# Kernel tuning notes

Hardware: AMD Instinct MI355X
Metric: run time of the kernel (lower is better)

The kernel has to match this reference:

```python
import jax, jax.numpy as jnp
import numpy as np

T, B, N = 12, 2, 1024
M = B * N            # nodes per timestep (batch-flattened)
D_IN, D_H, D_T, D_O = 64, 128, 16, 32


def _linear_params(k, fin, fout):
    kw, kb = jax.random.split(k)
    s = 1.0 / np.sqrt(fin)
    w = jax.random.uniform(kw, (fin, fout), jnp.float32, -s, s)
    b = jax.random.uniform(kb, (fout,), jnp.float32, -s, s)
    return w, b


def setup_inputs() -> dict:
    key = jax.random.key(0)
    ks = jax.random.split(key, 12)
    x = jax.random.normal(ks[0], (T, M, D_IN), jnp.float32)
    A = (jax.random.uniform(ks[1], (T, M, M)) < 0.01).astype(jnp.float32)
    A = A * (1.0 - jnp.eye(M, dtype=jnp.float32))  # no self-loops in raw adjacency
    ego_mask = jax.random.randint(ks[2], (B, T, N), 0, 2).astype(bool)
    gcn1_w, gcn1_b = _linear_params(ks[3], D_IN, D_H)
    gcn2_w, gcn2_b = _linear_params(ks[4], D_H, D_H)
    time_w, time_b = _linear_params(ks[5], 1, D_T)
    q_w, q_b = _linear_params(ks[6], D_H + D_T, D_H)
    k_w, k_b = _linear_params(ks[7], D_H + D_T, D_H)
    v_w, v_b = _linear_params(ks[8], D_H + D_T, D_H)
    o_w, o_b = _linear_params(ks[9], D_H, D_H)
    fc_w, fc_b = _linear_params(ks[10], D_H, D_O)
    return dict(x=x, A=A, ego_mask=ego_mask,
                gcn1_w=gcn1_w, gcn1_b=gcn1_b, gcn2_w=gcn2_w, gcn2_b=gcn2_b,
                time_w=time_w, time_b=time_b,
                q_w=q_w, q_b=q_b, k_w=k_w, k_b=k_b, v_w=v_w, v_b=v_b,
                o_w=o_w, o_b=o_b, fc_w=fc_w, fc_b=fc_b)


def _forward(x, A, ego_mask, gcn1_w, gcn1_b, gcn2_w, gcn2_b, time_w, time_b,
             q_w, q_b, k_w, k_b, v_w, v_b, o_w, o_b, fc_w, fc_b):
    # [B,T,N] -> [T, B*N], as in mask.permute(1,0,2).reshape(T,-1)
    mask = ego_mask.transpose(1, 0, 2).reshape(T, M)
    tvals = jnp.arange(T, dtype=jnp.float32)

    def step(_, inp):
        xt, At, mt, tv = inp  # [M,D_IN], [M,M], [M] bool, scalar
        m = mt.astype(xt.dtype)
        # restrict adjacency to masked subgraph; GCNConv adds self-loops
        A_hat = At * (m[:, None] * m[None, :]) + jnp.diag(m)
        deg = A_hat.sum(axis=0)  # in-degree per target (PyG gcn_norm on col)
        nrm = jnp.where(deg > 0, 1.0 / jnp.sqrt(jnp.maximum(deg, 1e-12)), 0.0)

        def gcn(h, w, b):
            # out[i] = nrm[i] * sum_j A_hat[j,i] * nrm[j] * (hW)[j] + b
            return (A_hat.T @ ((h @ w) * nrm[:, None])) * nrm[:, None] + b

        h = jax.nn.relu(gcn(xt, gcn1_w, gcn1_b))
        h = jax.nn.relu(gcn(h, gcn2_w, gcn2_b))
        # t_vec = sin(Linear(1,D_T)(t)) -- identical for all nodes
        t_vec = jnp.sin(tv * time_w[0] + time_b)  # [D_T]
        xtc = jnp.concatenate([h, jnp.broadcast_to(t_vec, (M, D_T))], axis=-1)
        Q = xtc @ q_w + q_b
        K = xtc @ k_w + k_b
        V = xtc @ v_w + v_b
        scores = (Q @ K.T) * (1.0 / np.sqrt(D_H))  # [M,M]
        scores = jnp.where(mt[None, :], scores, -1e9)  # keys restricted to mask
        agg = jax.nn.softmax(scores, axis=-1) @ V
        out = ((agg @ o_w + o_b) @ fc_w + fc_b) * m[:, None]  # scatter-back == mask
        return None, out

    _, outs = jax.lax.scan(step, None, (x, A, mask, tvals))  # [T,M,D_O]
    return outs.reshape(T, B, N, D_O).transpose(1, 2, 0, 3)  # [B,N,T,D_O]


def reference(x, A, ego_mask, gcn1_w, gcn1_b, gcn2_w, gcn2_b, time_w, time_b,
              q_w, q_b, k_w, k_b, v_w, v_b, o_w, o_b, fc_w, fc_b):
    return _forward(x, A, ego_mask, gcn1_w, gcn1_b, gcn2_w, gcn2_b, time_w,
                    time_b, q_w, q_b, k_w, k_b, v_w, v_b, o_w, o_b, fc_w, fc_b)
```

## Files before the change

kernel.cpp:

```cpp
#include <hip/hip_runtime.h>
#include <stdint.h>

#define TT   12
#define BB   2
#define NN   1024
#define MM   2048
#define TM   24576
#define DIN  64
#define DH   128
#define DOUT 32
#define CAP  64
#define NSPL 4

typedef __attribute__((ext_vector_type(8))) short short8;
typedef __attribute__((ext_vector_type(4))) short short4v;
typedef __attribute__((ext_vector_type(4))) float f32x4;

#define MFMA(a,b,c) __builtin_amdgcn_mfma_f32_16x16x32_bf16((a),(b),(c),0,0,0)

__device__ __forceinline__ float bf2f(unsigned short u){
  union { uint32_t i; float f; } x; x.i = ((uint32_t)u) << 16; return x.f;
}
__device__ __forceinline__ unsigned short f2bf(float f){
  union { float f; uint32_t i; } x; x.f = f;
  uint32_t u = x.i + 0x7FFFu + ((x.i >> 16) & 1u);
  return (unsigned short)(u >> 16);
}
__device__ __forceinline__ float LD(const void* p, size_t i, int mode){
  return mode ? ((const float*)p)[i] : bf2f(((const unsigned short*)p)[i]);
}

__global__ void k_fill(float* __restrict__ out, int n, float val){
  int i = blockIdx.x*blockDim.x + threadIdx.x;
  if(i < n) out[i] = val;
}

__global__ void k_dtype(const unsigned short* __restrict__ x, int* __restrict__ dtf,
                        int* __restrict__ nact){
  __shared__ int cnt_s;
  if(threadIdx.x==0) cnt_s = 0;
  if(threadIdx.x < TT) nact[threadIdx.x] = 0;
  __syncthreads();
  int c = 0;
  for(int i=threadIdx.x; i<6144; i+=blockDim.x){
    unsigned short h = x[i*2];
    unsigned e = (h >> 7) & 0xFF;
    if(h==0 || (e >= 0x60 && e <= 0x9F)) c++;
  }
  atomicAdd(&cnt_s, c);
  __syncthreads();
  if(threadIdx.x==0) *dtf = (cnt_s > 4000) ? 0 : 1;
}

__global__ void k_detect(const unsigned char* __restrict__ p, int* __restrict__ flag){
  __shared__ int pres_s, ge2_s;
  if(threadIdx.x==0){ pres_s=0; ge2_s=0; }
  __syncthreads();
  int pres=0, ge2=0;
  for(int i=threadIdx.x; i<24576; i+=blockDim.x){
    unsigned v = p[i];
    if(v){ pres |= 1 << (i & 7); if(v >= 2u) ge2 = 1; }
  }
  if(pres) atomicOr(&pres_s, pres);
  if(ge2)  atomicOr(&ge2_s, 1);
  __syncthreads();
  if(threadIdx.x==0){
    int pr = pres_s, g2 = ge2_s, mode;
    if(!g2){
      if((pr & ~0x01) == 0)      mode = 4;
      else if((pr & ~0x11) == 0) mode = 0;
      else                       mode = 1;
    } else {
      if((pr & ~0xC0) == 0)      mode = 5;
      else if((pr & ~0xCC) == 0) mode = 3;
      else                       mode = 2;
    }
    *flag = mode;
  }
}

__global__ void k_mask(const void* __restrict__ egom, const int* __restrict__ flag,
                       int* __restrict__ cnt, int* __restrict__ nact,
                       int* __restrict__ aidx, int* __restrict__ inv){
  int idx = blockIdx.x*blockDim.x + threadIdx.x;
  int t = idx / MM, node = idx % MM;
  int b = node / NN, n = node % NN;
  int src = (b*TT + t)*NN + n;
  int mode = *flag;
  int v;
  if(mode==0)      v = ((const int*)egom)[src] != 0;
  else if(mode==1) v = ((const unsigned char*)egom)[src] != 0;
  else if(mode==2) v = ((const unsigned short*)egom)[src] != 0;
  else if(mode==3) v = ((const float*)egom)[src] != 0.f;
  else if(mode==4) v = ((const long long*)egom)[src] != 0;
  else             v = ((const double*)egom)[src] != 0.0;
  cnt[idx] = 0;
  unsigned long long bal = __ballot(v != 0);
  int lane = threadIdx.x & 63;
  int base = 0;
  if(lane == 0 && bal) base = atomicAdd(&nact[t], __popcll(bal));
  base = __shfl(base, 0, 64);
  int ic = -1;
  if(v){
    int pfx = __popcll(bal & ((1ULL << lane) - 1ULL));
    ic = base + pfx;
    aidx[(size_t)t*MM + ic] = node;
  }
  inv[idx] = ic;
}

__global__ void k_conv(const void* __restrict__ x, const int* __restrict__ dtf,
                       const int* __restrict__ nact, const int* __restrict__ aidx,
                       unsigned short* __restrict__ xc){
  int id = blockIdx.x*blockDim.x + threadIdx.x;
  int rowc = id >> 3, seg = id & 7;
  int t = rowc / MM, ic = rowc % MM;
  int na = nact[t];
  if(ic >= ((na+63)&~63)) return;
  short8 o = {0,0,0,0,0,0,0,0};
  if(ic < na){
    int node = aidx[(size_t)t*MM + ic];
    size_t src = ((size_t)t*MM + node)*DIN + seg*8;
    if(*dtf){
      const float4* xf = (const float4*)((const float*)x + src);
      float4 a = xf[0], b = xf[1];
      o[0]=(short)f2bf(a.x); o[1]=(short)f2bf(a.y); o[2]=(short)f2bf(a.z); o[3]=(short)f2bf(a.w);
      o[4]=(short)f2bf(b.x); o[5]=(short)f2bf(b.y); o[6]=(short)f2bf(b.z); o[7]=(short)f2bf(b.w);
    } else {
      o = *(const short8*)((const unsigned short*)x + src);
    }
  }
  *(short8*)(xc + (size_t)rowc*DIN + seg*8) = o;
}

__global__ void k_prepw(
  const void* __restrict__ w1, const void* __restrict__ w2,
  const void* __restrict__ qw, const void* __restrict__ kw, const void* __restrict__ vw,
  const void* __restrict__ qb0, const void* __restrict__ kb0, const void* __restrict__ vb0,
  const void* __restrict__ ow, const void* __restrict__ ob,
  const void* __restrict__ fw, const void* __restrict__ fb,
  const void* __restrict__ tw, const void* __restrict__ tb,
  const void* __restrict__ b1, const void* __restrict__ b2,
  const int* __restrict__ dtf,
  unsigned short* __restrict__ W1t, unsigned short* __restrict__ W2t,
  unsigned short* __restrict__ Wqt, unsigned short* __restrict__ Wkt,
  unsigned short* __restrict__ Wvt, unsigned short* __restrict__ Wct,
  float* __restrict__ qbf, float* __restrict__ kbf, float* __restrict__ vbf,
  float* __restrict__ bcf, float* __restrict__ b1f, float* __restrict__ b2f)
{
  const int md = *dtf;
  int id = blockIdx.x*blockDim.x + threadIdx.x;
  if(id < 8192){ int n=id/64, k2=id%64; W1t[n*64+k2]=f2bf(LD(w1,(size_t)k2*128+n,md)); return; }
  id -= 8192;
  if(id < 16384){ int n=id/128,k2=id%128; W2t[n*128+k2]=f2bf(LD(w2,(size_t)k2*128+n,md)); return; }
  id -= 16384;
  if(id < 16384){ int n=id/128,k2=id%128; Wqt[n*128+k2]=f2bf(LD(qw,(size_t)k2*128+n,md)); return; }
  id -= 16384;
  if(id < 16384){ int n=id/128,k2=id%128; Wkt[n*128+k2]=f2bf(LD(kw,(size_t)k2*128+n,md)); return; }
  id -= 16384;
  if(id < 16384){ int n=id/128,k2=id%128; Wvt[n*128+k2]=f2bf(LD(vw,(size_t)k2*128+n,md)); return; }
  id -= 16384;
  if(id < 4096){
    int oc=id/128, c=id%128; float s=0.f;
    for(int r=0;r<128;r++) s += LD(ow,(size_t)c*128+r,md)*LD(fw,(size_t)r*32+oc,md);
    Wct[oc*128+c]=f2bf(s); return;
  }
  id -= 4096;
  if(id < 32){
    float s = LD(fb,id,md);
    for(int r=0;r<128;r++) s += LD(ob,r,md)*LD(fw,(size_t)r*32+id,md);
    bcf[id]=s; return;
  }
  id -= 32;
  if(id < 4608){
    int which = id/1536, rem=id%1536, t=rem/128, n=rem%128;
    const void* W  = which==0?qw:(which==1?kw:vw);
    const void* Bs = which==0?qb0:(which==1?kb0:vb0);
    float s = LD(Bs,n,md);
    for(int d=0;d<16;d++){
      float tv = sinf((float)t*LD(tw,d,md) + LD(tb,d,md));
      s += tv * LD(W,(size_t)(128+d)*128+n,md);
    }
    float* dst = which==0?qbf:(which==1?kbf:vbf);
    dst[t*128+n]=s; return;
  }
  id -= 4608;
  if(id < 256){
    if(id<128) b1f[id] = LD(b1,id,md);
    else       b2f[id-128] = LD(b2,id-128,md);
    return;
  }
}

__global__ __launch_bounds__(256) void k_edges(const void* __restrict__ A,
    const int* __restrict__ dtf, const int* __restrict__ inv,
    int* __restrict__ cnt, int* __restrict__ edges){
  int id = blockIdx.x*blockDim.x + threadIdx.x;
  int seg = id & 63; int row = id >> 6;
  int t = row / MM;
  int jc = inv[row];
  if(jc < 0) return;
  const int* invt = inv + (size_t)t*MM;
  int* cb = cnt + (size_t)t*MM;
  int* eb = edges + (size_t)t*MM*CAP;
  if(*dtf){
    const float4* p4 = (const float4*)((const float*)A + (size_t)row*MM + seg*32);
    #pragma unroll
    for(int u=0;u<8;u++){
      float4 v = p4[u];
      float wd[4]={v.x,v.y,v.z,v.w};
      #pragma unroll
      for(int q=0;q<4;q++){
        if(wd[q]!=0.f){
          int ibc = invt[seg*32 + u*4 + q];
          if(ibc >= 0){ int s=atomicAdd(&cb[ibc],1); if(s<CAP) eb[(size_t)ibc*CAP+s]=jc; }
        }
      }
    }
  } else {
    const uint4* p4 = (const uint4*)((const unsigned short*)A + (size_t)row*MM + seg*32);
    #pragma unroll
    for(int u=0;u<4;u++){
      uint4 v = p4[u];
      unsigned wd[4]={v.x,v.y,v.z,v.w};
      #pragma unroll
      for(int q=0;q<4;q++){
        int ib = seg*32 + u*8 + q*2;
        if(wd[q] & 0xFFFFu){
          int ibc = invt[ib];
          if(ibc >= 0){ int s=atomicAdd(&cb[ibc],1); if(s<CAP) eb[(size_t)ibc*CAP+s]=jc; }
        }
        if(wd[q] >> 16){
          int ibc = invt[ib+1];
          if(ibc >= 0){ int s=atomicAdd(&cb[ibc],1); if(s<CAP) eb[(size_t)ibc*CAP+s]=jc; }
        }
      }
    }
  }
}

template<int KD>
__global__ __launch_bounds__(256) void k_gemm_f32(const unsigned short* __restrict__ X,
    const unsigned short* __restrict__ Wt, float* __restrict__ g,
    const int* __restrict__ nact)
{
  constexpr int KS = KD/32;
  const int tile = blockIdx.x*64;
  const int t = tile / MM, il = tile % MM;
  const int na = nact[t];
  if(il >= ((na+63)&~63)) return;
  const int tid=threadIdx.x, wv=tid>>6, lane=tid&63, l15=lane&15, quad=lane>>4;
  const int r0 = tile + (wv>>1)*32;
  const int c0 = (wv&1)*64;
  short8 bf[KS][4];
  #pragma unroll
  for(int kk=0;kk<KS;kk++)
    #pragma unroll
    for(int nt=0;nt<4;nt++)
      bf[kk][nt] = *(const short8*)(Wt + (size_t)(c0+nt*16+l15)*KD + kk*32 + quad*8);
  f32x4 z = {0.f,0.f,0.f,0.f};
  f32x4 acc[2][4];
  #pragma unroll
  for(int i=0;i<2;i++){ acc[i][0]=z; acc[i][1]=z; acc[i][2]=z; acc[i][3]=z; }
  #pragma unroll
  for(int kk=0;kk<KS;kk++){
    short8 a0 = *(const short8*)(X + (size_t)(r0+l15)*KD    + kk*32 + quad*8);
    short8 a1 = *(const short8*)(X + (size_t)(r0+16+l15)*KD + kk*32 + quad*8);
    #pragma unroll
    for(int nt=0;nt<4;nt++){
      acc[0][nt]=MFMA(a0,bf[kk][nt],acc[0][nt]);
      acc[1][nt]=MFMA(a1,bf[kk][nt],acc[1][nt]);
    }
  }
  #pragma unroll
  for(int mt=0;mt<2;mt++)
    #pragma unroll
    for(int nt=0;nt<4;nt++){
      int col = c0+nt*16+l15;
      #pragma unroll
      for(int r=0;r<4;r++){
        int row = r0 + mt*16 + quad*4 + r;
        g[(size_t)row*DH + col] = acc[mt][nt][r];
      }
    }
}

__global__ __launch_bounds__(256) void k_gather(const float* __restrict__ g,
    const int* __restrict__ edges, const int* __restrict__ cnt,
    const int* __restrict__ nact, const float* __restrict__ bias,
    unsigned short* __restrict__ h)
{
  int wv = threadIdx.x>>6, lane = threadIdx.x&63;
  int gi = blockIdx.x*4 + wv;
  int t = gi / MM, ic = gi % MM;
  int na = nact[t];
  if(ic >= ((na+63)&~63)) return;
  if(ic >= na){
    h[(size_t)gi*DH + lane] = 0; h[(size_t)gi*DH + 64 + lane] = 0;
    return;
  }
  float a0=0.f, a1=0.f;
  int cn = cnt[gi]; if(cn>CAP) cn=CAP;
  const int* eb = edges + (size_t)gi*CAP;
  for(int e=0;e<cn;e++){
    int jc = eb[e];
    float nj = rsqrtf((float)cnt[(size_t)t*MM+jc] + 1.f);
    const float* gr = g + ((size_t)t*MM + jc)*DH;
    a0 += nj*gr[lane]; a1 += nj*gr[64+lane];
  }
  float ni = rsqrtf((float)cn + 1.f);
  const float* gs = g + (size_t)gi*DH;
  float h0 = ni*(a0 + ni*gs[lane])    + bias[lane];
  float h1 = ni*(a1 + ni*gs[64+lane]) + bias[64+lane];
  h0 = h0>0.f?h0:0.f; h1 = h1>0.f?h1:0.f;
  h[(size_t)gi*DH + lane]      = f2bf(h0);
  h[(size_t)gi*DH + 64 + lane] = f2bf(h1);
}

__global__ __launch_bounds__(256) void k_gemm_qkv(const unsigned short* __restrict__ X,
    const unsigned short* __restrict__ Wq, const unsigned short* __restrict__ Wk,
    const unsigned short* __restrict__ Wv,
    const float* __restrict__ qb, const float* __restrict__ kb, const float* __restrict__ vb,
    unsigned short* __restrict__ Qo, unsigned short* __restrict__ Ko,
    unsigned short* __restrict__ Vr, const int* __restrict__ nact)
{
  const int tile = blockIdx.x*64;
  const int t = tile / MM, il = tile % MM;
  const int na = nact[t];
  if(il >= ((na+63)&~63)) return;
  const int which = blockIdx.z;
  const unsigned short* Wt = which==0?Wq:(which==1?Wk:Wv);
  const float* bias = which==0?qb:(which==1?kb:vb);
  unsigned short* o = which==0?Qo:(which==1?Ko:Vr);
  const int tid=threadIdx.x, wv=tid>>6, lane=tid&63, l15=lane&15, quad=lane>>4;
  const int r0 = tile + (wv>>1)*32;
  const int c0 = (wv&1)*64;
  short8 bf[4][4];
  #pragma unroll
  for(int kk=0;kk<4;kk++)
    #pragma unroll
    for(int nt=0;nt<4;nt++)
      bf[kk][nt] = *(const short8*)(Wt + (size_t)(c0+nt*16+l15)*DH + kk*32 + quad*8);
  f32x4 z = {0.f,0.f,0.f,0.f};
  f32x4 acc[2][4];
  #pragma unroll
  for(int i=0;i<2;i++){ acc[i][0]=z; acc[i][1]=z; acc[i][2]=z; acc[i][3]=z; }
  #pragma unroll
  for(int kk=0;kk<4;kk++){
    short8 a0 = *(const short8*)(X + (size_t)(r0+l15)*DH    + kk*32 + quad*8);
    short8 a1 = *(const short8*)(X + (size_t)(r0+16+l15)*DH + kk*32 + quad*8);
    #pragma unroll
    for(int nt=0;nt<4;nt++){
      acc[0][nt]=MFMA(a0,bf[kk][nt],acc[0][nt]);
      acc[1][nt]=MFMA(a1,bf[kk][nt],acc[1][nt]);
    }
  }
  #pragma unroll
  for(int mt=0;mt<2;mt++)
    #pragma unroll
    for(int nt=0;nt<4;nt++){
      int col = c0+nt*16+l15;
      float bb = bias[t*DH+col];
      #pragma unroll
      for(int r=0;r<4;r++){
        int row = r0 + mt*16 + quad*4 + r;
        o[(size_t)row*DH + col] = f2bf(acc[mt][nt][r] + bb);
      }
    }
}

__global__ __launch_bounds__(64) void k_vtrans(const unsigned short* __restrict__ Vr,
    const int* __restrict__ nact, unsigned short* __restrict__ Vtc)
{
  __shared__ unsigned short tl[64][130];
  const int i0 = blockIdx.x*64, t = blockIdx.y, l = threadIdx.x;
  const int na = nact[t];
  if(i0 >= ((na+63)&~63)) return;
  for(int r=0;r<64;r++){
    uint32_t vv = *(const uint32_t*)(Vr + ((size_t)t*MM + i0 + r)*DH + 2*l);
    tl[r][2*l]   = (unsigned short)(vv & 0xFFFFu);
    tl[r][2*l+1] = (unsigned short)(vv >> 16);
  }
  __syncthreads();
  for(int c=0;c<DH;c++)
    Vtc[(size_t)t*DH*MM + (size_t)c*MM + i0 + l] = tl[l][c];
}

__global__ __launch_bounds__(64) void k_attn_split(
  const unsigned short* __restrict__ Q, const unsigned short* __restrict__ Kc,
  const unsigned short* __restrict__ Vtc, const int* __restrict__ nact,
  float* __restrict__ part, float* __restrict__ lpart)
{
  __shared__ short Pl[16][72];
  const int lane=threadIdx.x&63, l15=lane&15, quad=lane>>4;
  const int t = blockIdx.y;
  const int qbase = blockIdx.x*16;
  const int z = blockIdx.z;
  const float scale = 0.088388347648318447f;
  const int na = nact[t];
  if(qbase >= na) return;
  const int nkt = (na + 63) >> 6;
  const int chunk = (nkt + NSPL - 1) / NSPL;
  const int kt0 = z*chunk;
  int kt1 = kt0 + chunk; if(kt1 > nkt) kt1 = nkt;

  short8 bq[4];
  #pragma unroll
  for(int kk=0;kk<4;kk++)
    bq[kk] = *(const short8*)(Q + ((size_t)t*MM + qbase + l15)*DH + kk*32 + quad*8);

  f32x4 zz = {0.f,0.f,0.f,0.f};
  f32x4 accPV[8];
  #pragma unroll
  for(int i=0;i<8;i++) accPV[i]=zz;
  float l_run = 0.f;

  for(int kt=kt0; kt<kt1; kt++){
    const int key0 = kt*64;
    #pragma unroll
    for(int mt=0;mt<4;mt++){
      f32x4 s = zz;
      const unsigned short* Krow = Kc + ((size_t)t*MM + key0 + mt*16 + l15)*DH;
      #pragma unroll
      for(int kk=0;kk<4;kk++){
        short8 ak = *(const short8*)(Krow + kk*32 + quad*8);
        s = MFMA(ak, bq[kk], s);
      }
      short4v pk;
      #pragma unroll
      for(int r=0;r<4;r++){
        float sv = fminf(fmaxf(s[r]*scale, -15.f), 15.f);
        float valid = (key0 + mt*16 + quad*4 + r < na) ? 1.f : 0.f;
        float p = __expf(sv) * valid;
        pk[r] = (short)f2bf(p);
        l_run += bf2f((unsigned short)pk[r]);
      }
      *(short4v*)&Pl[l15][mt*16 + quad*4] = pk;
    }
    #pragma unroll
    for(int kk=0;kk<2;kk++){
      short8 ap = *(const short8*)&Pl[l15][kk*32 + quad*8];
      const unsigned short* Vb = Vtc + (size_t)t*DH*MM + key0 + kk*32 + quad*8;
      #pragma unroll
      for(int nt=0;nt<8;nt++){
        short8 bv = *(const short8*)(Vb + (size_t)(nt*16 + l15)*MM);
        accPV[nt] = MFMA(ap, bv, accPV[nt]);
      }
    }
  }
  l_run += __shfl_xor(l_run, 16, 64);
  l_run += __shfl_xor(l_run, 32, 64);

  const size_t pbase = (size_t)(z*TT + t)*MM + qbase;
  #pragma unroll
  for(int nt=0;nt<8;nt++)
    #pragma unroll
    for(int r=0;r<4;r++)
      part[(pbase + quad*4 + r)*128 + nt*16 + l15] = accPV[nt][r];
  if(lane < 16) lpart[pbase + lane] = l_run;
}

__global__ __launch_bounds__(64) void k_attn_fin(
  const float* __restrict__ part, const float* __restrict__ lpart,
  const int* __restrict__ aidx, const int* __restrict__ nact,
  const unsigned short* __restrict__ Wct, const float* __restrict__ bc,
  float* __restrict__ out)
{
  __shared__ short Al[16][136];
  __shared__ float lbuf[16];
  const int lane=threadIdx.x&63, l15=lane&15, quad=lane>>4;
  const int t = blockIdx.y, qbase = blockIdx.x*16;
  const int na = nact[t];
  if(qbase >= na) return;
  f32x4 acc4[8];
  f32x4 zz = {0.f,0.f,0.f,0.f};
  #pragma unroll
  for(int i=0;i<8;i++) acc4[i]=zz;
  #pragma unroll
  for(int s=0;s<NSPL;s++){
    const float* pb = part + ((size_t)(s*TT + t)*MM + qbase)*128;
    #pragma unroll
    for(int i=0;i<8;i++){
      int flat = i*64 + lane;
      int q = flat >> 5, c4 = (flat & 31) << 2;
      acc4[i] += *(const f32x4*)(pb + q*128 + c4);
    }
  }
  if(lane < 16){
    float ls = 0.f;
    #pragma unroll
    for(int s=0;s<NSPL;s++) ls += lpart[(size_t)(s*TT + t)*MM + qbase + lane];
    lbuf[lane] = ls;
  }
  #pragma unroll
  for(int i=0;i<8;i++){
    int flat = i*64 + lane;
    int q = flat >> 5, c4 = (flat & 31) << 2;
    short4v pk;
    #pragma unroll
    for(int r=0;r<4;r++){
      float av = fminf(fmaxf(acc4[i][r], -1e30f), 1e30f);
      pk[r] = (short)f2bf(av);
    }
    *(short4v*)&Al[q][c4] = pk;
  }
  __syncthreads();

  const int qc = qbase + l15;
  const bool qok = (qc < na);
  const float lsv = lbuf[l15];
  const float linv = (lsv > 0.f) ? 1.f/lsv : 0.f;
  const int node = aidx[(size_t)t*MM + (qok ? qc : 0)];
  #pragma unroll
  for(int mt2=0;mt2<2;mt2++){
    f32x4 d = zz;
    #pragma unroll
    for(int kk=0;kk<4;kk++){
      short8 aw = *(const short8*)(Wct + (size_t)(mt2*16+l15)*DH + kk*32 + quad*8);
      short8 bl = *(const short8*)&Al[l15][kk*32 + quad*8];
      d = MFMA(aw, bl, d);
    }
    f32x4 bcv = *(const f32x4*)(bc + mt2*16 + quad*4);
    f32x4 o4;
    #pragma unroll
    for(int r=0;r<4;r++) o4[r] = d[r]*linv + bcv[r];
    if(qok)
      *(f32x4*)(out + (size_t)node*(TT*DOUT) + (size_t)t*DOUT + mt2*16 + quad*4) = o4;
  }
}

extern "C" void kernel_launch(void* const* d_in, const int* in_sizes, int n_in,
                              void* d_out, int out_size, void* d_ws, size_t ws_size,
                              hipStream_t stream)
{
  float* outp = (float*)d_out;
  static const int EXP[19] = {1572864,50331648,24576,8192,128,16384,128,16,16,
                              18432,128,18432,128,18432,128,16384,128,4096,32};
  bool ok = (n_in >= 19) && (out_size == 786432);
  if(ok) for(int i=0;i<19;i++) if(in_sizes[i] != EXP[i]) { ok = false; break; }
  if(!ok){
    k_fill<<<(out_size+255)/256,256,0,stream>>>(outp, out_size, 1000.f);
    return;
  }
  const void* x   = d_in[0];
  const void* A   = d_in[1];
  const void* eg  = d_in[2];
  const void* w1  = d_in[3];
  const void* b1  = d_in[4];
  const void* w2  = d_in[5];
  const void* b2  = d_in[6];
  const void* tw  = d_in[7];
  const void* tb  = d_in[8];
  const void* qw  = d_in[9];
  const void* qb0 = d_in[10];
  const void* kw  = d_in[11];
  const void* kb0 = d_in[12];
  const void* vw  = d_in[13];
  const void* vb0 = d_in[14];
  const void* ow  = d_in[15];
  const void* ob  = d_in[16];
  const void* fw  = d_in[17];
  const void* fb  = d_in[18];

  char* w = (char*)d_ws;
  size_t off = 0;
  auto alloc = [&](size_t sz)->char*{
    char* p = w + off; off = (off + sz + 255) & ~(size_t)255; return p; };
  int*   flag  = (int*)  alloc(4);
  int*   dtf   = (int*)  alloc(4);
  int*   nactb = (int*)  alloc(TT*4);
  int*   cnt   = (int*)  alloc((size_t)TM*4);
  int*   aidx  = (int*)  alloc((size_t)TM*4);
  int*   inv   = (int*)  alloc((size_t)TM*4);
  int*   edges = (int*)  alloc((size_t)TM*CAP*4);
  float* g     = (float*)alloc((size_t)TM*DH*4);
  unsigned short* h   = (unsigned short*)alloc((size_t)TM*DH*2);
  unsigned short* xc  = (unsigned short*)alloc((size_t)TM*DIN*2);
  unsigned short* Vr  = (unsigned short*)alloc((size_t)TM*DH*2);
  unsigned short* Vtc = (unsigned short*)alloc((size_t)TT*DH*MM*2);
  unsigned short* W1t = (unsigned short*)alloc(DH*DIN*2);
  unsigned short* W2t = (unsigned short*)alloc(DH*DH*2);
  unsigned short* Wqt = (unsigned short*)alloc(DH*DH*2);
  unsigned short* Wkt = (unsigned short*)alloc(DH*DH*2);
  unsigned short* Wvt = (unsigned short*)alloc(DH*DH*2);
  unsigned short* Wct = (unsigned short*)alloc(DOUT*DH*2);
  float* qbf = (float*)alloc(TT*DH*4);
  float* kbf = (float*)alloc(TT*DH*4);
  float* vbf = (float*)alloc(TT*DH*4);
  float* bcf = (float*)alloc(DOUT*4);
  float* b1f = (float*)alloc(DH*4);
  float* b2f = (float*)alloc(DH*4);
  float* part  = (float*)alloc((size_t)NSPL*TM*DH*4);
  float* lpart = (float*)alloc((size_t)NSPL*TM*4);
  if(off > ws_size){
    k_fill<<<(out_size+255)/256,256,0,stream>>>(outp, out_size, 500.f);
    return;
  }

  unsigned short* Qb = (unsigned short*)g;
  unsigned short* Kb = (unsigned short*)((char*)g + (size_t)TM*DH*2);

  k_fill<<<(out_size+255)/256,256,0,stream>>>(outp, out_size, 0.f);
  k_dtype<<<1,256,0,stream>>>((const unsigned short*)x, dtf, nactb);
  k_detect<<<1,256,0,stream>>>((const unsigned char*)eg, flag);
  k_mask<<<TM/256,256,0,stream>>>(eg, flag, cnt, nactb, aidx, inv);
  k_conv<<<TM*8/256,256,0,stream>>>(x, dtf, nactb, aidx, xc);
  k_prepw<<<(82720+255)/256,256,0,stream>>>(w1,w2,qw,kw,vw,qb0,kb0,vb0,ow,ob,fw,fb,tw,tb,
                                            b1,b2,dtf,
                                            W1t,W2t,Wqt,Wkt,Wvt,Wct,qbf,kbf,vbf,bcf,b1f,b2f);
  k_edges<<<TM*64/256,256,0,stream>>>(A, dtf, inv, cnt, edges);
  k_gemm_f32<DIN><<<TM/64,256,0,stream>>>(xc, W1t, g, nactb);
  k_gather<<<TM/4,256,0,stream>>>(g, edges, cnt, nactb, b1f, h);
  k_gemm_f32<DH><<<TM/64,256,0,stream>>>(h, W2t, g, nactb);
  k_gather<<<TM/4,256,0,stream>>>(g, edges, cnt, nactb, b2f, h);
  k_gemm_qkv<<<dim3(TM/64,1,3),256,0,stream>>>(h, Wqt,Wkt,Wvt, qbf,kbf,vbf, Qb,Kb,Vr, nactb);
  k_vtrans<<<dim3(MM/64,TT),64,0,stream>>>(Vr, nactb, Vtc);
  k_attn_split<<<dim3(MM/16,TT,NSPL),64,0,stream>>>(Qb, Kb, Vtc, nactb, part, lpart);
  k_attn_fin<<<dim3(MM/16,TT),64,0,stream>>>(part, lpart, aidx, nactb, Wct, bcf, outp);
}
```

Measured before the change: 571.7 us.

## Fuse small prologue kernels and fold gather/transposes into GEMM loads and stores

Merges the dtype and mask-format detection kernels into one two-block launch, and folds the output zero-fill into the mask kernel. The compaction copy (k_conv) is removed by gathering x rows through aidx directly inside the first GEMM. The separate V transpose kernel is removed by having the QKV GEMM write V in transposed layout. The weight-prep index order is also changed so reads of the source weights coalesce. These cut several launches and intermediate buffers, at the cost of uncoalesced strided stores for the transposed V and gathered A-operand loads in the first GEMM.

```diff
diff --git a/kernel.cpp b/kernel.cpp
--- a/kernel.cpp
+++ b/kernel.cpp
@@ -11,6 +11,7 @@
 #define DOUT 32
 #define CAP  64
 #define NSPL 4
+#define OUTSZ 786432
 
 typedef __attribute__((ext_vector_type(8))) short short8;
 typedef __attribute__((ext_vector_type(4))) short short4v;
@@ -29,60 +30,76 @@
 __device__ __forceinline__ float LD(const void* p, size_t i, int mode){
   return mode ? ((const float*)p)[i] : bf2f(((const unsigned short*)p)[i]);
 }
+__device__ __forceinline__ short8 ldx8(const void* x, size_t off, int md){
+  if(md){
+    const float4* xf = (const float4*)((const float*)x + off);
+    float4 a = xf[0], b = xf[1];
+    short8 o;
+    o[0]=(short)f2bf(a.x); o[1]=(short)f2bf(a.y); o[2]=(short)f2bf(a.z); o[3]=(short)f2bf(a.w);
+    o[4]=(short)f2bf(b.x); o[5]=(short)f2bf(b.y); o[6]=(short)f2bf(b.z); o[7]=(short)f2bf(b.w);
+    return o;
+  }
+  return *(const short8*)((const unsigned short*)x + off);
+}
 
 __global__ void k_fill(float* __restrict__ out, int n, float val){
   int i = blockIdx.x*blockDim.x + threadIdx.x;
   if(i < n) out[i] = val;
 }
 
-__global__ void k_dtype(const unsigned short* __restrict__ x, int* __restrict__ dtf,
-                        int* __restrict__ nact){
-  __shared__ int cnt_s;
-  if(threadIdx.x==0) cnt_s = 0;
-  if(threadIdx.x < TT) nact[threadIdx.x] = 0;
-  __syncthreads();
-  int c = 0;
-  for(int i=threadIdx.x; i<6144; i+=blockDim.x){
-    unsigned short h = x[i*2];
-    unsigned e = (h >> 7) & 0xFF;
-    if(h==0 || (e >= 0x60 && e <= 0x9F)) c++;
-  }
-  atomicAdd(&cnt_s, c);
-  __syncthreads();
-  if(threadIdx.x==0) *dtf = (cnt_s > 4000) ? 0 : 1;
-}
-
-__global__ void k_detect(const unsigned char* __restrict__ p, int* __restrict__ flag){
-  __shared__ int pres_s, ge2_s;
-  if(threadIdx.x==0){ pres_s=0; ge2_s=0; }
-  __syncthreads();
-  int pres=0, ge2=0;
-  for(int i=threadIdx.x; i<24576; i+=blockDim.x){
-    unsigned v = p[i];
-    if(v){ pres |= 1 << (i & 7); if(v >= 2u) ge2 = 1; }
-  }
-  if(pres) atomicOr(&pres_s, pres);
-  if(ge2)  atomicOr(&ge2_s, 1);
-  __syncthreads();
-  if(threadIdx.x==0){
-    int pr = pres_s, g2 = ge2_s, mode;
-    if(!g2){
-      if((pr & ~0x01) == 0)      mode = 4;
-      else if((pr & ~0x11) == 0) mode = 0;
-      else                       mode = 1;
-    } else {
-      if((pr & ~0xC0) == 0)      mode = 5;
-      else if((pr & ~0xCC) == 0) mode = 3;
-      else                       mode = 2;
-    }
-    *flag = mode;
+__global__ void k_detect2(const unsigned short* __restrict__ x,
+                          const unsigned char* __restrict__ eg,
+                          int* __restrict__ dtf, int* __restrict__ flag,
+                          int* __restrict__ nact){
+  if(blockIdx.x == 0){
+    __shared__ int cnt_s;
+    if(threadIdx.x==0) cnt_s = 0;
+    if(threadIdx.x < TT) nact[threadIdx.x] = 0;
+    __syncthreads();
+    int c = 0;
+    for(int i=threadIdx.x; i<6144; i+=blockDim.x){
+      unsigned short h = x[i*2];
+      unsigned e = (h >> 7) & 0xFF;
+      if(h==0 || (e >= 0x60 && e <= 0x9F)) c++;
+    }
+    atomicAdd(&cnt_s, c);
+    __syncthreads();
+    if(threadIdx.x==0) *dtf = (cnt_s > 4000) ? 0 : 1;
+  } else {
+    __shared__ int pres_s, ge2_s;
+    if(threadIdx.x==0){ pres_s=0; ge2_s=0; }
+    __syncthreads();
+    int pres=0, ge2=0;
+    for(int i=threadIdx.x; i<24576; i+=blockDim.x){
+      unsigned v = eg[i];
+      if(v){ pres |= 1 << (i & 7); if(v >= 2u) ge2 = 1; }
+    }
+    if(pres) atomicOr(&pres_s, pres);
+    if(ge2)  atomicOr(&ge2_s, 1);
+    __syncthreads();
+    if(threadIdx.x==0){
+      int pr = pres_s, g2 = ge2_s, mode;
+      if(!g2){
+        if((pr & ~0x01) == 0)      mode = 4;
+        else if((pr & ~0x11) == 0) mode = 0;
+        else                       mode = 1;
+      } else {
+        if((pr & ~0xC0) == 0)      mode = 5;
+        else if((pr & ~0xCC) == 0) mode = 3;
+        else                       mode = 2;
+      }
+      *flag = mode;
+    }
   }
 }
 
 __global__ void k_mask(const void* __restrict__ egom, const int* __restrict__ flag,
                        int* __restrict__ cnt, int* __restrict__ nact,
-                       int* __restrict__ aidx, int* __restrict__ inv){
+                       int* __restrict__ aidx, int* __restrict__ inv,
+                       float* __restrict__ out){
   int idx = blockIdx.x*blockDim.x + threadIdx.x;
+  out[idx] = 0.f;
+  if(idx >= TM) return;
   int t = idx / MM, node = idx % MM;
   int b = node / NN, n = node % NN;
   int src = (b*TT + t)*NN + n;
@@ -109,30 +126,6 @@
   inv[idx] = ic;
 }
 
-__global__ void k_conv(const void* __restrict__ x, const int* __restrict__ dtf,
-                       const int* __restrict__ nact, const int* __restrict__ aidx,
-                       unsigned short* __restrict__ xc){
-  int id = blockIdx.x*blockDim.x + threadIdx.x;
-  int rowc = id >> 3, seg = id & 7;
-  int t = rowc / MM, ic = rowc % MM;
-  int na = nact[t];
-  if(ic >= ((na+63)&~63)) return;
-  short8 o = {0,0,0,0,0,0,0,0};
-  if(ic < na){
-    int node = aidx[(size_t)t*MM + ic];
-    size_t src = ((size_t)t*MM + node)*DIN + seg*8;
-    if(*dtf){
-      const float4* xf = (const float4*)((const float*)x + src);
-      float4 a = xf[0], b = xf[1];
-      o[0]=(short)f2bf(a.x); o[1]=(short)f2bf(a.y); o[2]=(short)f2bf(a.z); o[3]=(short)f2bf(a.w);
-      o[4]=(short)f2bf(b.x); o[5]=(short)f2bf(b.y); o[6]=(short)f2bf(b.z); o[7]=(short)f2bf(b.w);
-    } else {
-      o = *(const short8*)((const unsigned short*)x + src);
-    }
-  }
-  *(short8*)(xc + (size_t)rowc*DIN + seg*8) = o;
-}
-
 __global__ void k_prepw(
   const void* __restrict__ w1, const void* __restrict__ w2,
   const void* __restrict__ qw, const void* __restrict__ kw, const void* __restrict__ vw,
@@ -150,18 +143,19 @@
 {
   const int md = *dtf;
   int id = blockIdx.x*blockDim.x + threadIdx.x;
-  if(id < 8192){ int n=id/64, k2=id%64; W1t[n*64+k2]=f2bf(LD(w1,(size_t)k2*128+n,md)); return; }
+  if(id < 8192){
+    int n=id&127, k2=id>>7; W1t[n*64+k2]=f2bf(LD(w1,(size_t)k2*128+n,md)); return; }
   id -= 8192;
-  if(id < 16384){ int n=id/128,k2=id%128; W2t[n*128+k2]=f2bf(LD(w2,(size_t)k2*128+n,md)); return; }
+  if(id < 16384){ int n=id&127,k2=id>>7; W2t[n*128+k2]=f2bf(LD(w2,(size_t)k2*128+n,md)); return; }
   id -= 16384;
-  if(id < 16384){ int n=id/128,k2=id%128; Wqt[n*128+k2]=f2bf(LD(qw,(size_t)k2*128+n,md)); return; }
+  if(id < 16384){ int n=id&127,k2=id>>7; Wqt[n*128+k2]=f2bf(LD(qw,(size_t)k2*128+n,md)); return; }
   id -= 16384;
-  if(id < 16384){ int n=id/128,k2=id%128; Wkt[n*128+k2]=f2bf(LD(kw,(size_t)k2*128+n,md)); return; }
+  if(id < 16384){ int n=id&127,k2=id>>7; Wkt[n*128+k2]=f2bf(LD(kw,(size_t)k2*128+n,md)); return; }
   id -= 16384;
-  if(id < 16384){ int n=id/128,k2=id%128; Wvt[n*128+k2]=f2bf(LD(vw,(size_t)k2*128+n,md)); return; }
+  if(id < 16384){ int n=id&127,k2=id>>7; Wvt[n*128+k2]=f2bf(LD(vw,(size_t)k2*128+n,md)); return; }
   id -= 16384;
   if(id < 4096){
-    int oc=id/128, c=id%128; float s=0.f;
+    int oc=id&31, c=id>>5; float s=0.f;
     for(int r=0;r<128;r++) s += LD(ow,(size_t)c*128+r,md)*LD(fw,(size_t)r*32+oc,md);
     Wct[oc*128+c]=f2bf(s); return;
   }
@@ -239,12 +233,61 @@
   }
 }
 
-template<int KD>
-__global__ __launch_bounds__(256) void k_gemm_f32(const unsigned short* __restrict__ X,
+__global__ __launch_bounds__(256) void k_gemm_x(const void* __restrict__ x,
+    const int* __restrict__ dtf, const int* __restrict__ nact,
+    const int* __restrict__ aidx, const unsigned short* __restrict__ Wt,
+    float* __restrict__ g)
+{
+  const int tile = blockIdx.x*64;
+  const int t = tile / MM, il = tile % MM;
+  const int na = nact[t];
+  if(il >= ((na+63)&~63)) return;
+  const int md = *dtf;
+  const int tid=threadIdx.x, wv=tid>>6, lane=tid&63, l15=lane&15, quad=lane>>4;
+  const int r0 = tile + (wv>>1)*32;
+  const int c0 = (wv&1)*64;
+  short8 bf[2][4];
+  #pragma unroll
+  for(int kk=0;kk<2;kk++)
+    #pragma unroll
+    for(int nt=0;nt<4;nt++)
+      bf[kk][nt] = *(const short8*)(Wt + (size_t)(c0+nt*16+l15)*DIN + kk*32 + quad*8);
+  const int il0 = (r0 % MM) + l15, il1 = (r0 % MM) + 16 + l15;
+  const int n0 = aidx[(size_t)t*MM + (il0 < na ? il0 : 0)];
+  const int n1 = aidx[(size_t)t*MM + (il1 < na ? il1 : 0)];
+  const size_t xb0 = ((size_t)t*MM + n0)*DIN;
+  const size_t xb1 = ((size_t)t*MM + n1)*DIN;
+  f32x4 z = {0.f,0.f,0.f,0.f};
+  f32x4 acc[2][4];
+  #pragma unroll
+  for(int i=0;i<2;i++){ acc[i][0]=z; acc[i][1]=z; acc[i][2]=z; acc[i][3]=z; }
+  #pragma unroll
+  for(int kk=0;kk<2;kk++){
+    short8 a0 = ldx8(x, xb0 + kk*32 + quad*8, md);
+    short8 a1 = ldx8(x, xb1 + kk*32 + quad*8, md);
+    #pragma unroll
+    for(int nt=0;nt<4;nt++){
+      acc[0][nt]=MFMA(a0,bf[kk][nt],acc[0][nt]);
+      acc[1][nt]=MFMA(a1,bf[kk][nt],acc[1][nt]);
+    }
+  }
+  #pragma unroll
+  for(int mt=0;mt<2;mt++)
+    #pragma unroll
+    for(int nt=0;nt<4;nt++){
+      int col = c0+nt*16+l15;
+      #pragma unroll
+      for(int r=0;r<4;r++){
+        int row = r0 + mt*16 + quad*4 + r;
+        g[(size_t)row*DH + col] = acc[mt][nt][r];
+      }
+    }
+}
+
+__global__ __launch_bounds__(256) void k_gemm_h(const unsigned short* __restrict__ X,
     const unsigned short* __restrict__ Wt, float* __restrict__ g,
     const int* __restrict__ nact)
 {
-  constexpr int KS = KD/32;
   const int tile = blockIdx.x*64;
   const int t = tile / MM, il = tile % MM;
   const int na = nact[t];
@@ -252,20 +295,20 @@
   const int tid=threadIdx.x, wv=tid>>6, lane=tid&63, l15=lane&15, quad=lane>>4;
   const int r0 = tile + (wv>>1)*32;
   const int c0 = (wv&1)*64;
-  short8 bf[KS][4];
-  #pragma unroll
-  for(int kk=0;kk<KS;kk++)
+  short8 bf[4][4];
+  #pragma unroll
+  for(int kk=0;kk<4;kk++)
     #pragma unroll
     for(int nt=0;nt<4;nt++)
-      bf[kk][nt] = *(const short8*)(Wt + (size_t)(c0+nt*16+l15)*KD + kk*32 + quad*8);
+      bf[kk][nt] = *(const short8*)(Wt + (size_t)(c0+nt*16+l15)*DH + kk*32 + quad*8);
   f32x4 z = {0.f,0.f,0.f,0.f};
   f32x4 acc[2][4];
   #pragma unroll
   for(int i=0;i<2;i++){ acc[i][0]=z; acc[i][1]=z; acc[i][2]=z; acc[i][3]=z; }
   #pragma unroll
-  for(int kk=0;kk<KS;kk++){
-    short8 a0 = *(const short8*)(X + (size_t)(r0+l15)*KD    + kk*32 + quad*8);
-    short8 a1 = *(const short8*)(X + (size_t)(r0+16+l15)*KD + kk*32 + quad*8);
+  for(int kk=0;kk<4;kk++){
+    short8 a0 = *(const short8*)(X + (size_t)(r0+l15)*DH    + kk*32 + quad*8);
+    short8 a1 = *(const short8*)(X + (size_t)(r0+16+l15)*DH + kk*32 + quad*8);
     #pragma unroll
     for(int nt=0;nt<4;nt++){
       acc[0][nt]=MFMA(a0,bf[kk][nt],acc[0][nt]);
@@ -322,7 +365,7 @@
     const unsigned short* __restrict__ Wv,
     const float* __restrict__ qb, const float* __restrict__ kb, const float* __restrict__ vb,
     unsigned short* __restrict__ Qo, unsigned short* __restrict__ Ko,
-    unsigned short* __restrict__ Vr, const int* __restrict__ nact)
+    unsigned short* __restrict__ Vtc, const int* __restrict__ nact)
 {
   const int tile = blockIdx.x*64;
   const int t = tile / MM, il = tile % MM;
@@ -331,7 +374,6 @@
   const int which = blockIdx.z;
   const unsigned short* Wt = which==0?Wq:(which==1?Wk:Wv);
   const float* bias = which==0?qb:(which==1?kb:vb);
-  unsigned short* o = which==0?Qo:(which==1?Ko:Vr);
   const int tid=threadIdx.x, wv=tid>>6, lane=tid&63, l15=lane&15, quad=lane>>4;
   const int r0 = tile + (wv>>1)*32;
   const int c0 = (wv&1)*64;
@@ -355,35 +397,34 @@
       acc[1][nt]=MFMA(a1,bf[kk][nt],acc[1][nt]);
     }
   }
-  #pragma unroll
-  for(int mt=0;mt<2;mt++)
-    #pragma unroll
-    for(int nt=0;nt<4;nt++){
-      int col = c0+nt*16+l15;
-      float bb = bias[t*DH+col];
-      #pragma unroll
-      for(int r=0;r<4;r++){
-        int row = r0 + mt*16 + quad*4 + r;
-        o[(size_t)row*DH + col] = f2bf(acc[mt][nt][r] + bb);
-      }
-    }
-}
-
-__global__ __launch_bounds__(64) void k_vtrans(const unsigned short* __restrict__ Vr,
-    const int* __restrict__ nact, unsigned short* __restrict__ Vtc)
-{
-  __shared__ unsigned short tl[64][130];
-  const int i0 = blockIdx.x*64, t = blockIdx.y, l = threadIdx.x;
-  const int na = nact[t];
-  if(i0 >= ((na+63)&~63)) return;
-  for(int r=0;r<64;r++){
-    uint32_t vv = *(const uint32_t*)(Vr + ((size_t)t*MM + i0 + r)*DH + 2*l);
-    tl[r][2*l]   = (unsigned short)(vv & 0xFFFFu);
-    tl[r][2*l+1] = (unsigned short)(vv >> 16);
-  }
-  __syncthreads();
-  for(int c=0;c<DH;c++)
-    Vtc[(size_t)t*DH*MM + (size_t)c*MM + i0 + l] = tl[l][c];
+  if(which < 2){
+    unsigned short* o = which==0 ? Qo : Ko;
+    #pragma unroll
+    for(int mt=0;mt<2;mt++)
+      #pragma unroll
+      for(int nt=0;nt<4;nt++){
+        int col = c0+nt*16+l15;
+        float bb = bias[t*DH+col];
+        #pragma unroll
+        for(int r=0;r<4;r++){
+          int row = r0 + mt*16 + quad*4 + r;
+          o[(size_t)row*DH + col] = f2bf(acc[mt][nt][r] + bb);
+        }
+      }
+  } else {
+    #pragma unroll
+    for(int mt=0;mt<2;mt++)
+      #pragma unroll
+      for(int nt=0;nt<4;nt++){
+        int col = c0+nt*16+l15;
+        float bb = bias[t*DH+col];
+        int node0 = il + (wv>>1)*32 + mt*16 + quad*4;
+        short4v pk;
+        #pragma unroll
+        for(int r=0;r<4;r++) pk[r] = (short)f2bf(acc[mt][nt][r] + bb);
+        *(short4v*)(Vtc + ((size_t)t*DH + col)*MM + node0) = pk;
+      }
+  }
 }
 
 __global__ __launch_bounds__(64) void k_attn_split(
@@ -536,7 +577,7 @@
   float* outp = (float*)d_out;
   static const int EXP[19] = {1572864,50331648,24576,8192,128,16384,128,16,16,
                               18432,128,18432,128,18432,128,16384,128,4096,32};
-  bool ok = (n_in >= 19) && (out_size == 786432);
+  bool ok = (n_in >= 19) && (out_size == OUTSZ);
   if(ok) for(int i=0;i<19;i++) if(in_sizes[i] != EXP[i]) { ok = false; break; }
   if(!ok){
     k_fill<<<(out_size+255)/256,256,0,stream>>>(outp, out_size, 1000.f);
@@ -575,8 +616,6 @@
   int*   edges = (int*)  alloc((size_t)TM*CAP*4);
   float* g     = (float*)alloc((size_t)TM*DH*4);
   unsigned short* h   = (unsigned short*)alloc((size_t)TM*DH*2);
-  unsigned short* xc  = (unsigned short*)alloc((size_t)TM*DIN*2);
-  unsigned short* Vr  = (unsigned short*)alloc((size_t)TM*DH*2);
   unsigned short* Vtc = (unsigned short*)alloc((size_t)TT*DH*MM*2);
   unsigned short* W1t = (unsigned short*)alloc(DH*DIN*2);
   unsigned short* W2t = (unsigned short*)alloc(DH*DH*2);
@@ -600,21 +639,18 @@
   unsigned short* Qb = (unsigned short*)g;
   unsigned short* Kb = (unsigned short*)((char*)g + (size_t)TM*DH*2);
 
-  k_fill<<<(out_size+255)/256,256,0,stream>>>(outp, out_size, 0.f);
-  k_dtype<<<1,256,0,stream>>>((const unsigned short*)x, dtf, nactb);
-  k_detect<<<1,256,0,stream>>>((const unsigned char*)eg, flag);
-  k_mask<<<TM/256,256,0,stream>>>(eg, flag, cnt, nactb, aidx, inv);
-  k_conv<<<TM*8/256,256,0,stream>>>(x, dtf, nactb, aidx, xc);
+  k_detect2<<<2,256,0,stream>>>((const unsigned short*)x, (const unsigned char*)eg,
+                                dtf, flag, nactb);
+  k_mask<<<OUTSZ/256,256,0,stream>>>(eg, flag, cnt, nactb, aidx, inv, outp);
   k_prepw<<<(82720+255)/256,256,0,stream>>>(w1,w2,qw,kw,vw,qb0,kb0,vb0,ow,ob,fw,fb,tw,tb,
                                             b1,b2,dtf,
                                             W1t,W2t,Wqt,Wkt,Wvt,Wct,qbf,kbf,vbf,bcf,b1f,b2f);
   k_edges<<<TM*64/256,256,0,stream>>>(A, dtf, inv, cnt, edges);
-  k_gemm_f32<DIN><<<TM/64,256,0,stream>>>(xc, W1t, g, nactb);
+  k_gemm_x<<<TM/64,256,0,stream>>>(x, dtf, nactb, aidx, W1t, g);
   k_gather<<<TM/4,256,0,stream>>>(g, edges, cnt, nactb, b1f, h);
-  k_gemm_f32<DH><<<TM/64,256,0,stream>>>(h, W2t, g, nactb);
+  k_gemm_h<<<TM/64,256,0,stream>>>(h, W2t, g, nactb);
   k_gather<<<TM/4,256,0,stream>>>(g, edges, cnt, nactb, b2f, h);
-  k_gemm_qkv<<<dim3(TM/64,1,3),256,0,stream>>>(h, Wqt,Wkt,Wvt, qbf,kbf,vbf, Qb,Kb,Vr, nactb);
-  k_vtrans<<<dim3(MM/64,TT),64,0,stream>>>(Vr, nactb, Vtc);
+  k_gemm_qkv<<<dim3(TM/64,1,3),256,0,stream>>>(h, Wqt,Wkt,Wvt, qbf,kbf,vbf, Qb,Kb,Vtc, nactb);
   k_attn_split<<<dim3(MM/16,TT,NSPL),64,0,stream>>>(Qb, Kb, Vtc, nactb, part, lpart);
   k_attn_fin<<<dim3(MM/16,TT),64,0,stream>>>(part, lpart, aidx, nactb, Wct, bcf, outp);
 }
```

Result: no change. 562.3 us (-1.6%).
